# Optimization experiments

Measured on AMD Instinct MI355X. Metric: run time of the kernel, lower is better.

## Reference

```python
import jax, jax.numpy as jnp
import numpy as np

N = 1048576      # batch of 3D points
NT = 8           # n_transforms
HID = 64         # hidden_dim
NB = 12          # num_bins
TB = 5.0         # tail_bound
MINW = 1e-3
MINH = 1e-3
MIND = 1e-3
OUT_DIM = 2 * NB * 3 + 2   # 74, per repo's out_features formula (37 per transformed feature)
DCONST = float(np.log(np.exp(1.0 - MIND) - 1.0))  # softplus^-1(1 - min_derivative)
LOGZ = -0.5 * 3.0 * float(np.log(2.0 * np.pi))


def setup_inputs() -> dict:
    key = jax.random.key(0)
    k = jax.random.split(key, 7)
    x = jax.random.normal(k[0], (N, 3), jnp.float32)
    # ResidualNet params per coupling layer (stacked over NT layers):
    W_in = jax.random.normal(k[1], (NT, HID, 1)) * 0.5
    b_in = jax.random.normal(k[2], (NT, HID)) * 0.1
    W_blk = jax.random.normal(k[3], (NT, 4, HID, HID)) * (1.0 / np.sqrt(HID))
    b_blk = jax.random.normal(k[4], (NT, 4, HID)) * 0.1
    W_out = jax.random.normal(k[5], (NT, OUT_DIM, HID)) * 0.1
    b_out = jax.random.normal(k[6], (NT, OUT_DIM)) * 0.1
    return dict(x=x, W_in=W_in, b_in=b_in, W_blk=W_blk, b_blk=b_blk,
                W_out=W_out, b_out=b_out)


def _knots(unnorm, min_size):
    # softmax -> min-width floor -> cumulative knot positions on [-TB, TB]
    sizes = jax.nn.softmax(unnorm, axis=-1)
    sizes = min_size + (1.0 - min_size * NB) * sizes
    cum = jnp.cumsum(sizes, axis=-1)
    cum = jnp.pad(cum, ((0, 0), (0, 0), (1, 0)))
    cum = 2.0 * TB * cum - TB
    cum = cum.at[..., 0].set(-TB).at[..., -1].set(TB)
    return cum, cum[..., 1:] - cum[..., :-1]


def _rq_spline(x, uw, uh, ud):
    # x: [N,2]; uw,uh: [N,2,NB]; ud: [N,2,NB+1]  (extra derivative param, as in repo)
    inside = (x >= -TB) & (x <= TB)
    xc = jnp.clip(x, -TB, TB)
    cw, widths = _knots(uw, MINW)
    ch, heights = _knots(uh, MINH)
    ud_p = jnp.pad(ud, ((0, 0), (0, 0), (1, 1)), constant_values=DCONST)
    d = MIND + jax.nn.softplus(ud_p)   # [N,2,NB+3]; knots 0..NB used
    # searchsorted: sum(x >= edges) - 1, with eps on last edge (nflows convention)
    cw_s = cw.at[..., -1].add(1e-6)
    bin_idx = jnp.sum((xc[..., None] >= cw_s).astype(jnp.int32), axis=-1) - 1
    bin_idx = jnp.clip(bin_idx, 0, NB - 1)
    idx = bin_idx[..., None]

    def g(a, i):
        return jnp.take_along_axis(a, i, axis=-1)[..., 0]

    in_cw = g(cw, idx)
    in_w = g(widths, idx)
    in_ch = g(ch, idx)
    in_h = g(heights, idx)
    delta = in_h / in_w
    d_k = g(d, idx)
    d_k1 = g(d, idx + 1)

    theta = (xc - in_cw) / in_w
    t1m = theta * (1.0 - theta)
    numerator = in_h * (delta * theta * theta + d_k * t1m)
    denominator = delta + (d_k + d_k1 - 2.0 * delta) * t1m
    y = in_ch + numerator / denominator
    dnum = (delta * delta) * (d_k1 * theta * theta + 2.0 * delta * t1m
                              + d_k * (1.0 - theta) ** 2)
    lad = jnp.log(dnum) - 2.0 * jnp.log(denominator)
    return jnp.where(inside, y, x), jnp.where(inside, lad, 0.0)


def reference(x, W_in, b_in, W_blk, b_blk, W_out, b_out):
    z = x
    lad_total = jnp.zeros(x.shape[0], x.dtype)
    for i in range(NT):
        z = z[:, ::-1]                       # ReversePermutation(features=3)
        ident, tr = z[:, :1], z[:, 1:]       # mask [0,1,1]: feat 0 identity, 1&2 transformed
        # ResidualNet: initial linear, 2 pre-activation residual blocks, final linear
        h = ident @ W_in[i].T + b_in[i]
        for j in range(2):
            t = jax.nn.relu(h) @ W_blk[i, 2 * j].T + b_blk[i, 2 * j]
            t = jax.nn.relu(t) @ W_blk[i, 2 * j + 1].T + b_blk[i, 2 * j + 1]
            h = h + t
        params = (h @ W_out[i].T + b_out[i]).reshape(-1, 2, 3 * NB + 1)
        uw = params[..., :NB]
        uh = params[..., NB:2 * NB]
        ud = params[..., 2 * NB:]
        tr_new, lad = _rq_spline(tr, uw, uh, ud)
        lad_total = lad_total + lad.sum(axis=-1)
        z = jnp.concatenate([ident, tr_new], axis=1)
    return -0.5 * jnp.sum(z * z, axis=-1) + LOGZ + lad_total
```

## Files before the change

kernel.cpp:

```cpp
#include <hip/hip_runtime.h>
#include <math.h>

namespace {

constexpr int   NT_   = 8;
constexpr int   NB_   = 12;
constexpr float TB_   = 5.0f;
constexpr float MINW_ = 0.001f;
constexpr float MINH_ = 0.001f;
constexpr float MIND_ = 0.001f;
constexpr float LOGZ_ = -2.7568155996140185f;

constexpr int PPP_   = 41;
constexpr int WAVES_ = 4;

constexpr int WT_DENSE_F = 32 * 4096;
constexpr int HEAD_FB    = WT_DENSE_F;
constexpr int WT_HEAD_F  = 8 * 5120;
constexpr int PREP_TOT_F = WT_DENSE_F + WT_HEAD_F;

constexpr int P2B_       = 131072;
constexpr int WT_P2      = 32 * 2048;
constexpr int HEAD_PB    = P2B_ + WT_P2;
constexpr int HP2B_      = HEAD_PB + WT_HEAD_F;
constexpr int WT_HP2     = 8 * 2560;
constexpr int PREP_TOT_P = HP2B_ + WT_HP2;
constexpr size_t WS_P_BYTES = (size_t)PREP_TOT_P * 4;

typedef __attribute__((ext_vector_type(8))) short        bf16x8;
typedef __attribute__((ext_vector_type(4))) float        f32x4;
typedef __attribute__((ext_vector_type(4))) unsigned int u32x4;

__device__ __forceinline__ float softplus_(float v) {
    return fmaxf(v, 0.0f) + log1pf(__expf(-fabsf(v)));
}

__device__ __forceinline__ void rq_spline_reg(const float (&p)[37], float xr,
                                              float& y_out, float& lad_out) {
    float mw = -1e30f, mh = -1e30f;
#pragma unroll
    for (int q = 0; q < NB_; ++q) { mw = fmaxf(mw, p[q]); mh = fmaxf(mh, p[NB_ + q]); }

    float ew[NB_], eh[NB_];
    float sw = 0.0f, sh = 0.0f;
#pragma unroll
    for (int q = 0; q < NB_; ++q) { ew[q] = __expf(p[q] - mw);        sw += ew[q]; }
#pragma unroll
    for (int q = 0; q < NB_; ++q) { eh[q] = __expf(p[NB_ + q] - mh);  sh += eh[q]; }

    const float iw = (1.0f - MINW_ * (float)NB_) / sw;
    const float ih = (1.0f - MINH_ * (float)NB_) / sh;

    float cw[NB_ + 1], ch[NB_ + 1];
    cw[0] = -TB_; ch[0] = -TB_;
    float rw = 0.0f, rh = 0.0f;
#pragma unroll
    for (int q = 0; q < NB_; ++q) {
        rw += MINW_ + ew[q] * iw;
        rh += MINH_ + eh[q] * ih;
        cw[q + 1] = fmaf(2.0f * TB_, rw, -TB_);
        ch[q + 1] = fmaf(2.0f * TB_, rh, -TB_);
    }
    cw[NB_] = TB_;
    ch[NB_] = TB_;

    const float xc = fminf(fmaxf(xr, -TB_), TB_);

    int bi = 0;
#pragma unroll
    for (int q = 1; q <= NB_ - 1; ++q) bi += (xc >= cw[q]) ? 1 : 0;

    float in_cw = cw[0], cwn = cw[1], in_ch = ch[0], chn = ch[1];
    float udm1 = 0.0f, ud0 = p[24];
#pragma unroll
    for (int q = 1; q < NB_; ++q) {
        const bool s = (bi == q);
        in_cw = s ? cw[q]         : in_cw;
        cwn   = s ? cw[q + 1]     : cwn;
        in_ch = s ? ch[q]         : in_ch;
        chn   = s ? ch[q + 1]     : chn;
        udm1  = s ? p[24 + q - 1] : udm1;
        ud0   = s ? p[24 + q]     : ud0;
    }
    const float in_w = cwn - in_cw;
    const float in_h = chn - in_ch;
    const float d_k  = (bi == 0) ? 1.0f : (MIND_ + softplus_(udm1));
    const float d_k1 = MIND_ + softplus_(ud0);

    const float delta = in_h / in_w;
    const float theta = (xc - in_cw) / in_w;
    const float omt   = 1.0f - theta;
    const float t1m   = theta * omt;
    const float num   = in_h * (delta * theta * theta + d_k * t1m);
    const float den   = delta + (d_k + d_k1 - 2.0f * delta) * t1m;
    const float y     = in_ch + num / den;
    const float dnum  = delta * delta * (d_k1 * theta * theta + 2.0f * delta * t1m + d_k * omt * omt);
    const float lad   = __logf(dnum) - 2.0f * __logf(den);

    const bool inside = (xr >= -TB_) && (xr <= TB_);
    y_out   = inside ? y   : xr;
    lad_out = inside ? lad : 0.0f;
}

__device__ __forceinline__ float trunc16_(float x) {
    return __uint_as_float(__float_as_uint(x) & 0xFFFF0000u);
}
__device__ __forceinline__ unsigned hi16_(float x) { return __float_as_uint(x) >> 16; }

__device__ __forceinline__ int head_param_(int ctg, int c) {
    if (ctg < 2)  return ctg * 16 + c;
    if (ctg >= 3) return 37 + (ctg - 3) * 16 + c;
    if (c < 5)                 return 32 + c;
    if (c >= 8 && c < 13)      return 69 + (c - 8);
    return -1;
}

__global__ __launch_bounds__(256) void prep_F(const float* __restrict__ Wb,
                                              const float* __restrict__ Wo,
                                              float* __restrict__ wt) {
    const int t = blockIdx.x * 256 + threadIdx.x;
    if (t >= PREP_TOT_F) return;
    if (t < WT_DENSE_F) {
        const int L   = t >> 12;
        const int rem = t & 4095;
        const int o   = rem >> 6;
        const int q   = (rem >> 2) & 15;
        const int k   = ((q ^ (o & 15)) << 2) | (rem & 3);
        wt[t] = Wb[((size_t)L * 64 + o) * 64 + k];
    } else {
        const int t2  = t - WT_DENSE_F;
        const int i   = t2 / 5120;
        const int r1  = t2 - i * 5120;
        const int ctg = r1 >> 10;
        const int rem = r1 & 1023;
        const int c   = rem >> 6;
        const int q   = (rem >> 2) & 15;
        const int k   = ((q ^ c) << 2) | (rem & 3);
        const int param = head_param_(ctg, c);
        wt[t] = (param >= 0) ? Wo[((size_t)i * 74 + param) * 64 + k] : 0.0f;
    }
}

__global__ __launch_bounds__(256) void prep_P(const float* __restrict__ Wb,
                                              const float* __restrict__ Wo,
                                              float* __restrict__ wt) {
    const int t = blockIdx.x * 256 + threadIdx.x;
    if (t >= PREP_TOT_P) return;
    unsigned* wtu = (unsigned*)wt;
    if (t < WT_DENSE_F) {
        const int L   = t >> 12;
        const int rem = t & 4095;
        const int o   = rem >> 6;
        const int q   = (rem >> 2) & 15;
        const int k   = ((q ^ (o & 15)) << 2) | (rem & 3);
        const float x  = Wb[((size_t)L * 64 + o) * 64 + k];
        wtu[t] = (hi16_(x) << 16) | hi16_(x - trunc16_(x));
    } else if (t < HEAD_PB) {
        const int t2   = t - P2B_;
        const int L    = t2 >> 11;
        const int rem  = t2 & 2047;
        const int g    = rem >> 8;
        const int ct   = g >> 1, ks = g & 1;
        const int r    = rem & 255;
        const int lane = r >> 2, j = r & 3;
        const int o    = ct * 16 + (lane & 15);
        const int kb   = 32 * ks + 8 * (lane >> 4) + 2 * j;
        const float x0 = Wb[((size_t)L * 64 + o) * 64 + kb];
        const float x1 = Wb[((size_t)L * 64 + o) * 64 + kb + 1];
        const float a0 = x0 - trunc16_(x0), b0 = a0 - trunc16_(a0);
        const float a1 = x1 - trunc16_(x1), b1 = a1 - trunc16_(a1);
        wtu[t] = (hi16_(b1) << 16) | hi16_(b0);
    } else if (t < HP2B_) {
        const int t2  = t - HEAD_PB;
        const int i   = t2 / 5120;
        const int r1  = t2 - i * 5120;
        const int ctg = r1 >> 10;
        const int rem = r1 & 1023;
        const int c   = rem >> 6;
        const int q   = (rem >> 2) & 15;
        const int k   = ((q ^ c) << 2) | (rem & 3);
        const int param = head_param_(ctg, c);
        const float x = (param >= 0) ? Wo[((size_t)i * 74 + param) * 64 + k] : 0.0f;
        wtu[t] = (hi16_(x) << 16) | hi16_(x - trunc16_(x));
    } else {
        const int t2   = t - HP2B_;
        const int i    = t2 / 2560;
        const int r1   = t2 - i * 2560;
        const int ctg  = r1 >> 9;
        const int r2   = r1 & 511;
        const int ks   = r2 >> 8;
        const int r    = r2 & 255;
        const int lane = r >> 2, j = r & 3;
        const int c    = lane & 15;
        const int kb   = 32 * ks + 8 * (lane >> 4) + 2 * j;
        const int param = head_param_(ctg, c);
        float x0 = 0.0f, x1 = 0.0f;
        if (param >= 0) {
            x0 = Wo[((size_t)i * 74 + param) * 64 + kb];
            x1 = Wo[((size_t)i * 74 + param) * 64 + kb + 1];
        }
        const float a0 = x0 - trunc16_(x0), b0 = a0 - trunc16_(a0);
        const float a1 = x1 - trunc16_(x1), b1 = a1 - trunc16_(a1);
        wtu[t] = (hi16_(b1) << 16) | hi16_(b0);
    }
}

template <int NC>
__device__ __forceinline__ void stage_(const float* __restrict__ g, float* lds,
                                       int wave, int wl) {
#pragma unroll
    for (int c = 0; c < (NC + WAVES_ - 1) / WAVES_; ++c) {
        const int cc = wave + WAVES_ * c;
        if (cc < NC) {
            __builtin_amdgcn_global_load_lds(
                (const __attribute__((address_space(1))) void*)(g + cc * 256 + wl * 4),
                (__attribute__((address_space(3))) void*)(lds + cc * 256), 16, 0, 0);
        }
    }
}

__device__ __forceinline__ f32x4 mfma16(u32x4 a, u32x4 b, f32x4 c) {
    return __builtin_amdgcn_mfma_f32_16x16x32_bf16(
        __builtin_bit_cast(bf16x8, a), __builtin_bit_cast(bf16x8, b), c, 0, 0, 0);
}

__device__ __forceinline__ u32x4 packhi8(const float (&v)[8]) {
    u32x4 r;
    r.x = __builtin_amdgcn_perm(__float_as_uint(v[1]), __float_as_uint(v[0]), 0x07060302u);
    r.y = __builtin_amdgcn_perm(__float_as_uint(v[3]), __float_as_uint(v[2]), 0x07060302u);
    r.z = __builtin_amdgcn_perm(__float_as_uint(v[5]), __float_as_uint(v[4]), 0x07060302u);
    r.w = __builtin_amdgcn_perm(__float_as_uint(v[7]), __float_as_uint(v[6]), 0x07060302u);
    return r;
}

__device__ __forceinline__ void split3_8(const float (&xv)[8],
                                         u32x4& f0, u32x4& f1, u32x4& f2) {
    float r1[8], r2[8];
#pragma unroll
    for (int j = 0; j < 8; ++j) r1[j] = xv[j] - trunc16_(xv[j]);
#pragma unroll
    for (int j = 0; j < 8; ++j) r2[j] = r1[j] - trunc16_(r1[j]);
    f0 = packhi8(xv);
    f1 = packhi8(r1);
    f2 = packhi8(r2);
}

__device__ __forceinline__ void load3(const float* __restrict__ base, int tbase,
                                      int r1, int r2, u32x4& f0, u32x4& f1, u32x4& f2) {
    const f32x4 q0 = *(const f32x4*)&base[tbase + r1];
    const f32x4 q1 = *(const f32x4*)&base[tbase + r2];
    const float xv[8] = {q0.x, q0.y, q0.z, q0.w, q1.x, q1.y, q1.z, q1.w};
    split3_8(xv, f0, f1, f2);
}

__device__ __forceinline__ void unpack01(const unsigned* __restrict__ WsU, int tbase,
                                         int r1, int r2, u32x4& b0, u32x4& b1) {
    const u32x4 d0 = *(const u32x4*)&WsU[tbase + r1];
    const u32x4 d1 = *(const u32x4*)&WsU[tbase + r2];
    b0.x = __builtin_amdgcn_perm(d0.y, d0.x, 0x07060302u);
    b0.y = __builtin_amdgcn_perm(d0.w, d0.z, 0x07060302u);
    b0.z = __builtin_amdgcn_perm(d1.y, d1.x, 0x07060302u);
    b0.w = __builtin_amdgcn_perm(d1.w, d1.z, 0x07060302u);
    b1.x = __builtin_amdgcn_perm(d0.y, d0.x, 0x05040100u);
    b1.y = __builtin_amdgcn_perm(d0.w, d0.z, 0x05040100u);
    b1.z = __builtin_amdgcn_perm(d1.y, d1.x, 0x05040100u);
    b1.w = __builtin_amdgcn_perm(d1.w, d1.z, 0x05040100u);
}

__device__ __forceinline__ void loadA_all(const float* __restrict__ slab,
                                          const int (&R1v)[2], const int (&R2v)[2],
                                          u32x4 (&a0)[4][2], u32x4 (&a1)[4][2],
                                          u32x4 (&a2)[4][2]) {
#pragma unroll
    for (int ks = 0; ks < 2; ++ks)
#pragma unroll
        for (int rt = 0; rt < 4; ++rt)
            load3(slab, rt * 1024, R1v[ks], R2v[ks],
                  a0[rt][ks], a1[rt][ks], a2[rt][ks]);
}

__device__ __forceinline__ void chain6(const u32x4& A0, const u32x4& A1, const u32x4& A2,
                                       const u32x4& b0, const u32x4& b1, const u32x4& b2,
                                       f32x4& a) {
    a = mfma16(A0, b2, a);
    a = mfma16(A2, b0, a);
    a = mfma16(A1, b1, a);
    a = mfma16(A1, b0, a);
    a = mfma16(A0, b1, a);
    a = mfma16(A0, b0, a);
}

__device__ __forceinline__ void gemm_ct_F(const float* __restrict__ Ws, int ct,
                                          const u32x4 (&a0)[4][2], const u32x4 (&a1)[4][2],
                                          const u32x4 (&a2)[4][2],
                                          const int (&R1v)[2], const int (&R2v)[2],
                                          f32x4 (&acc)[4]) {
#pragma unroll
    for (int ks = 0; ks < 2; ++ks) {
        u32x4 b0, b1, b2;
        load3(Ws, ct * 1024, R1v[ks], R2v[ks], b0, b1, b2);
#pragma unroll
        for (int rt = 0; rt < 4; ++rt)
            chain6(a0[rt][ks], a1[rt][ks], a2[rt][ks], b0, b1, b2, acc[rt]);
    }
}

__device__ __forceinline__ void gemm_ct_P(const unsigned* __restrict__ WsU, int ct,
                                          const u32x4 (&a0)[4][2], const u32x4 (&a1)[4][2],
                                          const u32x4 (&a2)[4][2],
                                          const int (&R1v)[2], const int (&R2v)[2],
                                          const unsigned* __restrict__ p2t,
                                          f32x4 (&acc)[4]) {
    u32x4 b2[2];
#pragma unroll
    for (int ks = 0; ks < 2; ++ks)
        b2[ks] = *(const u32x4*)(p2t + ks * 256);
#pragma unroll
    for (int ks = 0; ks < 2; ++ks) {
        u32x4 b0, b1;
        unpack01(WsU, ct * 1024, R1v[ks], R2v[ks], b0, b1);
#pragma unroll
        for (int rt = 0; rt < 4; ++rt)
            chain6(a0[rt][ks], a1[rt][ks], a2[rt][ks], b0, b1, b2[ks], acc[rt]);
    }
}

template <bool P, bool RESID, bool RELU_OUT>
__device__ __forceinline__ void dense_layer(
    float* __restrict__ slab, const float* __restrict__ Ws,
    const u32x4 (&a0)[4][2], const u32x4 (&a1)[4][2], const u32x4 (&a2)[4][2],
    const int (&R1v)[2], const int (&R2v)[2],
    const unsigned* __restrict__ p2,
    const float* __restrict__ bias_g, float (&hreg)[4][4][4],
    const int (&K1)[4], const int (&K2)[4], int l15)
{
    const unsigned* WsU = (const unsigned*)Ws;
    float bly[4];
#pragma unroll
    for (int ct = 0; ct < 4; ++ct) bly[ct] = bias_g[ct * 16 + l15];
#pragma unroll
    for (int ct = 0; ct < 4; ++ct) {
        f32x4 acc[4];
#pragma unroll
        for (int rt = 0; rt < 4; ++rt) {
            if (RESID)
                acc[rt] = f32x4{hreg[rt][ct][0] + bly[ct], hreg[rt][ct][1] + bly[ct],
                                hreg[rt][ct][2] + bly[ct], hreg[rt][ct][3] + bly[ct]};
            else
                acc[rt] = f32x4{bly[ct], bly[ct], bly[ct], bly[ct]};
        }
        if constexpr (P)
            gemm_ct_P(WsU, ct, a0, a1, a2, R1v, R2v, p2 + ct * 512, acc);
        else
            gemm_ct_F(Ws, ct, a0, a1, a2, R1v, R2v, acc);
#pragma unroll
        for (int rt = 0; rt < 4; ++rt) {
            if (RESID) {
#pragma unroll
                for (int r = 0; r < 4; ++r) hreg[rt][ct][r] = acc[rt][r];
            }
            const int base = rt * 1024 + K2[ct];
#pragma unroll
            for (int r = 0; r < 4; ++r) {
                const float v = RELU_OUT ? fmaxf(acc[rt][r], 0.0f) : acc[rt][r];
                slab[base + K1[r]] = v;
            }
        }
    }
}

template <bool P>
__device__ __forceinline__ void head_ct(const float* __restrict__ Ws, int ct,
                                        const u32x4 (&a0)[4][2], const u32x4 (&a1)[4][2],
                                        const u32x4 (&a2)[4][2],
                                        const int (&R1v)[2], const int (&R2v)[2],
                                        const unsigned* __restrict__ hp2, int ctg,
                                        f32x4 (&acc)[4]) {
    if constexpr (P)
        gemm_ct_P((const unsigned*)Ws, ct, a0, a1, a2, R1v, R2v, hp2 + ctg * 512, acc);
    else
        gemm_ct_F(Ws, ct, a0, a1, a2, R1v, R2v, acc);
}

template <bool P>
__global__ __launch_bounds__(256, 2) void nsf_kernel(
    const float* __restrict__ x,
    const float* __restrict__ W_in,  const float* __restrict__ b_in,
    const float* __restrict__ b_blk, const float* __restrict__ b_out,
    const float* __restrict__ wt,
    float* __restrict__ out, int n)
{
    __shared__ __align__(16) float As2[WAVES_ * 4096];
    __shared__ __align__(16) float Ws[4096];

    constexpr int HB = P ? HEAD_PB : HEAD_FB;

    const int l    = threadIdx.x;
    const int wave = l >> 6;
    const int wl   = l & 63;
    const int l15  = wl & 15;
    const int lhi  = wl >> 4;
    float* slab = As2 + wave * 4096;

    const int gidx = blockIdx.x * 256 + l;
    const int idx  = gidx < n ? gidx : (n - 1);

    float z0 = x[3 * idx + 0];
    float z1 = x[3 * idx + 1];
    float z2 = x[3 * idx + 2];
    float lad_total = 0.0f;

    int K1[4], K2[4], R1v[2], R2v[2], P1[4];
#pragma unroll
    for (int r = 0; r < 4; ++r)
        K1[r] = (4 * lhi + r) * 64 + ((((l15 >> 2) ^ r)) << 2) + (l15 & 3);
#pragma unroll
    for (int c = 0; c < 4; ++c) K2[c] = (c ^ lhi) << 4;
#pragma unroll
    for (int s = 0; s < 2; ++s) {
        const int c0 = 8 * s + 2 * lhi;
        R1v[s] = l15 * 64 + ((c0 ^ l15) << 2);
        R2v[s] = l15 * 64 + (((c0 + 1) ^ l15) << 2);
    }
#pragma unroll
    for (int r = 0; r < 4; ++r) P1[r] = (4 * lhi + r) * PPP_ + l15;

    const unsigned* p2w  = (const unsigned*)wt + P2B_  + wl * 4;
    const unsigned* hp2w = (const unsigned*)wt + HP2B_ + wl * 4;

    stage_<16>(wt, Ws, wave, wl);
    __syncthreads();

#pragma unroll 1
    for (int i = 0; i < NT_; ++i) {
        const float ident = z2, tr0 = z1, tr1 = z0;
        const unsigned* hp2 = hp2w + (size_t)i * 2560;

        u32x4 a0[4][2], a1[4][2], a2[4][2];
        float hreg[4][4][4];
        {
            float idA[4], idD[4][4];
#pragma unroll
            for (int rt = 0; rt < 4; ++rt) idA[rt] = __shfl(ident, 16 * rt + l15, 64);
#pragma unroll
            for (int rt = 0; rt < 4; ++rt)
#pragma unroll
                for (int r = 0; r < 4; ++r)
                    idD[rt][r] = __shfl(ident, 16 * rt + 4 * lhi + r, 64);
#pragma unroll
            for (int ks = 0; ks < 2; ++ks) {
                const int kb = i * 64 + 32 * ks + 8 * lhi;
                const f32x4 w0 = *(const f32x4*)&W_in[kb];
                const f32x4 w1 = *(const f32x4*)&W_in[kb + 4];
                const f32x4 c0 = *(const f32x4*)&b_in[kb];
                const f32x4 c1 = *(const f32x4*)&b_in[kb + 4];
                const float wv[8] = {w0.x, w0.y, w0.z, w0.w, w1.x, w1.y, w1.z, w1.w};
                const float bv[8] = {c0.x, c0.y, c0.z, c0.w, c1.x, c1.y, c1.z, c1.w};
#pragma unroll
                for (int rt = 0; rt < 4; ++rt) {
                    float hx[8];
#pragma unroll
                    for (int j = 0; j < 8; ++j)
                        hx[j] = fmaxf(fmaf(idA[rt], wv[j], bv[j]), 0.0f);
                    split3_8(hx, a0[rt][ks], a1[rt][ks], a2[rt][ks]);
                }
            }
#pragma unroll
            for (int ct = 0; ct < 4; ++ct) {
                const float wD = W_in[i * 64 + ct * 16 + l15];
                const float bD = b_in[i * 64 + ct * 16 + l15];
#pragma unroll
                for (int rt = 0; rt < 4; ++rt)
#pragma unroll
                    for (int r = 0; r < 4; ++r)
                        hreg[rt][ct][r] = fmaf(idD[rt][r], wD, bD);
            }
        }

        dense_layer<P, false, true>(slab, Ws, a0, a1, a2, R1v, R2v,
                                    p2w + (size_t)(i * 4 + 0) * 2048,
                                    b_blk + (size_t)(i * 4 + 0) * 64, hreg, K1, K2, l15);
        __syncthreads();
        stage_<16>(wt + (size_t)(i * 4 + 1) * 4096, Ws, wave, wl);
        loadA_all(slab, R1v, R2v, a0, a1, a2);
        __syncthreads();

        dense_layer<P, true, true>(slab, Ws, a0, a1, a2, R1v, R2v,
                                   p2w + (size_t)(i * 4 + 1) * 2048,
                                   b_blk + (size_t)(i * 4 + 1) * 64, hreg, K1, K2, l15);
        __syncthreads();
        stage_<16>(wt + (size_t)(i * 4 + 2) * 4096, Ws, wave, wl);
        loadA_all(slab, R1v, R2v, a0, a1, a2);
        __syncthreads();

        dense_layer<P, false, true>(slab, Ws, a0, a1, a2, R1v, R2v,
                                    p2w + (size_t)(i * 4 + 2) * 2048,
                                    b_blk + (size_t)(i * 4 + 2) * 64, hreg, K1, K2, l15);
        __syncthreads();
        stage_<16>(wt + (size_t)(i * 4 + 3) * 4096, Ws, wave, wl);
        loadA_all(slab, R1v, R2v, a0, a1, a2);
        __syncthreads();

        dense_layer<P, true, false>(slab, Ws, a0, a1, a2, R1v, R2v,
                                    p2w + (size_t)(i * 4 + 3) * 2048,
                                    b_blk + (size_t)(i * 4 + 3) * 64, hreg, K1, K2, l15);
        __syncthreads();
        stage_<12>(wt + HB + (size_t)i * 5120, Ws, wave, wl);
        loadA_all(slab, R1v, R2v, a0, a1, a2);
        __syncthreads();

        f32x4 combD[4];
#pragma unroll
        for (int ct = 0; ct < 3; ++ct) {
            f32x4 acc[4];
#pragma unroll
            for (int rt = 0; rt < 4; ++rt) acc[rt] = f32x4{0.f, 0.f, 0.f, 0.f};
            head_ct<P>(Ws, ct, a0, a1, a2, R1v, R2v, hp2, ct, acc);
            if (ct < 2) {
#pragma unroll
                for (int rt = 0; rt < 4; ++rt)
#pragma unroll
                    for (int r = 0; r < 4; ++r)
                        slab[rt * 656 + P1[r] + 16 * ct] = acc[rt][r];
            } else {
#pragma unroll
                for (int rt = 0; rt < 4; ++rt) combD[rt] = acc[rt];
                if (l15 < 5) {
#pragma unroll
                    for (int rt = 0; rt < 4; ++rt)
#pragma unroll
                        for (int r = 0; r < 4; ++r)
                            slab[rt * 656 + P1[r] + 32] = acc[rt][r];
                }
            }
        }
        __syncthreads();
        stage_<8>(wt + HB + (size_t)i * 5120 + 3072, Ws, wave, wl);

        const float* bo = b_out + i * 74;
        float y0, l0v, y1, l1v;
        {
            float p0[37];
#pragma unroll
            for (int q = 0; q < 37; ++q) p0[q] = slab[wl * PPP_ + q] + bo[q];
            rq_spline_reg(p0, tr0, y0, l0v);
        }
        __syncthreads();

#pragma unroll
        for (int ct = 0; ct < 2; ++ct) {
            f32x4 acc[4];
#pragma unroll
            for (int rt = 0; rt < 4; ++rt) acc[rt] = f32x4{0.f, 0.f, 0.f, 0.f};
            head_ct<P>(Ws, ct, a0, a1, a2, R1v, R2v, hp2, 3 + ct, acc);
#pragma unroll
            for (int rt = 0; rt < 4; ++rt)
#pragma unroll
                for (int r = 0; r < 4; ++r)
                    slab[rt * 656 + P1[r] + 16 * ct] = acc[rt][r];
        }
        if (l15 >= 8 && l15 < 13) {
#pragma unroll
            for (int rt = 0; rt < 4; ++rt)
#pragma unroll
                for (int r = 0; r < 4; ++r)
                    slab[rt * 656 + P1[r] + 24] = combD[rt][r];
        }
        __syncthreads();
        if (i < NT_ - 1) stage_<16>(wt + (size_t)((i + 1) * 4) * 4096, Ws, wave, wl);
        {
            float p1[37];
#pragma unroll
            for (int q = 0; q < 37; ++q) p1[q] = slab[wl * PPP_ + q] + bo[37 + q];
            rq_spline_reg(p1, tr1, y1, l1v);
        }
        __syncthreads();

        lad_total += l0v + l1v;
        z0 = ident;
        z1 = y0;
        z2 = y1;
    }

    if (gidx < n)
        out[gidx] = -0.5f * (z0 * z0 + z1 * z1 + z2 * z2) + LOGZ_ + lad_total;
}

}

extern "C" void kernel_launch(void* const* d_in, const int* in_sizes, int n_in,
                              void* d_out, int out_size, void* d_ws, size_t ws_size,
                              hipStream_t stream) {
    const float* x     = (const float*)d_in[0];
    const float* W_in  = (const float*)d_in[1];
    const float* b_in  = (const float*)d_in[2];
    const float* W_blk = (const float*)d_in[3];
    const float* b_blk = (const float*)d_in[4];
    const float* W_out = (const float*)d_in[5];
    const float* b_out = (const float*)d_in[6];
    float* out = (float*)d_out;

    const int n = in_sizes[0] / 3;
    const int grid = (n + 255) / 256;

    if (ws_size >= WS_P_BYTES) {
        prep_P<<<(PREP_TOT_P + 255) / 256, 256, 0, stream>>>(
            W_blk, W_out, (float*)d_ws);
        nsf_kernel<true><<<grid, 256, 0, stream>>>(x, W_in, b_in, b_blk, b_out,
                                                   (const float*)d_ws, out, n);
    } else {
        prep_F<<<(PREP_TOT_F + 255) / 256, 256, 0, stream>>>(
            W_blk, W_out, (float*)d_ws);
        nsf_kernel<false><<<grid, 256, 0, stream>>>(x, W_in, b_in, b_blk, b_out,
                                                    (const float*)d_ws, out, n);
    }
}
```

Measured before the change: 1.880 ms.

## Read MFMA B-fragments directly from global in per-lane layout, drop LDS weight staging

The packed weight path is reorganised so the dense and head weights are pre-permuted into per-lane fragment order. Each wave then loads its B operands straight from global memory (L2-cached), so the LDS weight staging and block-wide barriers go away. The kernel becomes single-wave blocks (64 threads, launch_bounds 64,3) with a per-wave LDS slab, which can raise occupancy and remove synchronisation. The trade-off is more global/L2 traffic for weights, since each wave re-reads them instead of sharing them through LDS.

```diff
diff --git a/kernel.cpp b/kernel.cpp
--- a/kernel.cpp
+++ b/kernel.cpp
@@ -141,18 +141,24 @@
     }
 }
 
-__global__ __launch_bounds__(256) void prep_P(const float* __restrict__ Wb,
+__global__ __launch_bounds__(256) void prep_G(const float* __restrict__ Wb,
                                               const float* __restrict__ Wo,
                                               float* __restrict__ wt) {
     const int t = blockIdx.x * 256 + threadIdx.x;
     if (t >= PREP_TOT_P) return;
     unsigned* wtu = (unsigned*)wt;
     if (t < WT_DENSE_F) {
-        const int L   = t >> 12;
-        const int rem = t & 4095;
-        const int o   = rem >> 6;
-        const int q   = (rem >> 2) & 15;
-        const int k   = ((q ^ (o & 15)) << 2) | (rem & 3);
+        const int L    = t >> 12;
+        const int rem  = t & 4095;
+        const int ct   = rem >> 10;
+        const int r2   = rem & 1023;
+        const int ks   = r2 >> 9;
+        const int r3   = r2 & 511;
+        const int half = r3 >> 8;
+        const int r4   = r3 & 255;
+        const int lane = r4 >> 2, m = r4 & 3;
+        const int o    = ct * 16 + (lane & 15);
+        const int k    = ks * 32 + (lane >> 4) * 8 + half * 4 + m;
         const float x  = Wb[((size_t)L * 64 + o) * 64 + k];
         wtu[t] = (hi16_(x) << 16) | hi16_(x - trunc16_(x));
     } else if (t < HEAD_PB) {
@@ -171,14 +177,18 @@
         const float a1 = x1 - trunc16_(x1), b1 = a1 - trunc16_(a1);
         wtu[t] = (hi16_(b1) << 16) | hi16_(b0);
     } else if (t < HP2B_) {
-        const int t2  = t - HEAD_PB;
-        const int i   = t2 / 5120;
-        const int r1  = t2 - i * 5120;
-        const int ctg = r1 >> 10;
-        const int rem = r1 & 1023;
-        const int c   = rem >> 6;
-        const int q   = (rem >> 2) & 15;
-        const int k   = ((q ^ c) << 2) | (rem & 3);
+        const int t2   = t - HEAD_PB;
+        const int i    = t2 / 5120;
+        const int r1   = t2 - i * 5120;
+        const int ctg  = r1 >> 10;
+        const int r2   = r1 & 1023;
+        const int ks   = r2 >> 9;
+        const int r3   = r2 & 511;
+        const int half = r3 >> 8;
+        const int r4   = r3 & 255;
+        const int lane = r4 >> 2, m = r4 & 3;
+        const int c    = lane & 15;
+        const int k    = ks * 32 + (lane >> 4) * 8 + half * 4 + m;
         const int param = head_param_(ctg, c);
         const float x = (param >= 0) ? Wo[((size_t)i * 74 + param) * 64 + k] : 0.0f;
         wtu[t] = (hi16_(x) << 16) | hi16_(x - trunc16_(x));
@@ -253,10 +263,8 @@
     split3_8(xv, f0, f1, f2);
 }
 
-__device__ __forceinline__ void unpack01(const unsigned* __restrict__ WsU, int tbase,
-                                         int r1, int r2, u32x4& b0, u32x4& b1) {
-    const u32x4 d0 = *(const u32x4*)&WsU[tbase + r1];
-    const u32x4 d1 = *(const u32x4*)&WsU[tbase + r2];
+__device__ __forceinline__ void unpack01r(const u32x4& d0, const u32x4& d1,
+                                          u32x4& b0, u32x4& b1) {
     b0.x = __builtin_amdgcn_perm(d0.y, d0.x, 0x07060302u);
     b0.y = __builtin_amdgcn_perm(d0.w, d0.z, 0x07060302u);
     b0.z = __builtin_amdgcn_perm(d1.y, d1.x, 0x07060302u);
@@ -305,36 +313,37 @@
     }
 }
 
-__device__ __forceinline__ void gemm_ct_P(const unsigned* __restrict__ WsU, int ct,
+__device__ __forceinline__ void gemm_ct_G(const unsigned* __restrict__ p01t,
+                                          const unsigned* __restrict__ p2t,
                                           const u32x4 (&a0)[4][2], const u32x4 (&a1)[4][2],
                                           const u32x4 (&a2)[4][2],
-                                          const int (&R1v)[2], const int (&R2v)[2],
-                                          const unsigned* __restrict__ p2t,
                                           f32x4 (&acc)[4]) {
-    u32x4 b2[2];
-#pragma unroll
-    for (int ks = 0; ks < 2; ++ks)
-        b2[ks] = *(const u32x4*)(p2t + ks * 256);
+    u32x4 d0[2], d1[2], c2[2];
+#pragma unroll
+    for (int ks = 0; ks < 2; ++ks) {
+        d0[ks] = *(const u32x4*)(p01t + ks * 512);
+        d1[ks] = *(const u32x4*)(p01t + ks * 512 + 256);
+        c2[ks] = *(const u32x4*)(p2t + ks * 256);
+    }
 #pragma unroll
     for (int ks = 0; ks < 2; ++ks) {
         u32x4 b0, b1;
-        unpack01(WsU, ct * 1024, R1v[ks], R2v[ks], b0, b1);
+        unpack01r(d0[ks], d1[ks], b0, b1);
 #pragma unroll
         for (int rt = 0; rt < 4; ++rt)
-            chain6(a0[rt][ks], a1[rt][ks], a2[rt][ks], b0, b1, b2[ks], acc[rt]);
-    }
-}
-
-template <bool P, bool RESID, bool RELU_OUT>
-__device__ __forceinline__ void dense_layer(
-    float* __restrict__ slab, const float* __restrict__ Ws,
+            chain6(a0[rt][ks], a1[rt][ks], a2[rt][ks], b0, b1, c2[ks], acc[rt]);
+    }
+}
+
+template <bool RESID, bool RELU_OUT>
+__device__ __forceinline__ void dense_layer_G(
+    float* __restrict__ slab,
     const u32x4 (&a0)[4][2], const u32x4 (&a1)[4][2], const u32x4 (&a2)[4][2],
-    const int (&R1v)[2], const int (&R2v)[2],
+    const unsigned* __restrict__ p01,
     const unsigned* __restrict__ p2,
     const float* __restrict__ bias_g, float (&hreg)[4][4][4],
     const int (&K1)[4], const int (&K2)[4], int l15)
 {
-    const unsigned* WsU = (const unsigned*)Ws;
     float bly[4];
 #pragma unroll
     for (int ct = 0; ct < 4; ++ct) bly[ct] = bias_g[ct * 16 + l15];
@@ -349,10 +358,7 @@
             else
                 acc[rt] = f32x4{bly[ct], bly[ct], bly[ct], bly[ct]};
         }
-        if constexpr (P)
-            gemm_ct_P(WsU, ct, a0, a1, a2, R1v, R2v, p2 + ct * 512, acc);
-        else
-            gemm_ct_F(Ws, ct, a0, a1, a2, R1v, R2v, acc);
+        gemm_ct_G(p01 + ct * 1024, p2 + ct * 512, a0, a1, a2, acc);
 #pragma unroll
         for (int rt = 0; rt < 4; ++rt) {
             if (RESID) {
@@ -369,21 +375,233 @@
     }
 }
 
-template <bool P>
-__device__ __forceinline__ void head_ct(const float* __restrict__ Ws, int ct,
-                                        const u32x4 (&a0)[4][2], const u32x4 (&a1)[4][2],
-                                        const u32x4 (&a2)[4][2],
-                                        const int (&R1v)[2], const int (&R2v)[2],
-                                        const unsigned* __restrict__ hp2, int ctg,
-                                        f32x4 (&acc)[4]) {
-    if constexpr (P)
-        gemm_ct_P((const unsigned*)Ws, ct, a0, a1, a2, R1v, R2v, hp2 + ctg * 512, acc);
-    else
+__device__ __forceinline__ void h_init_(int i, float ident, int l15, int lhi,
+                                        const float* __restrict__ W_in,
+                                        const float* __restrict__ b_in,
+                                        u32x4 (&a0)[4][2], u32x4 (&a1)[4][2],
+                                        u32x4 (&a2)[4][2], float (&hreg)[4][4][4]) {
+    float idA[4], idD[4][4];
+#pragma unroll
+    for (int rt = 0; rt < 4; ++rt) idA[rt] = __shfl(ident, 16 * rt + l15, 64);
+#pragma unroll
+    for (int rt = 0; rt < 4; ++rt)
+#pragma unroll
+        for (int r = 0; r < 4; ++r)
+            idD[rt][r] = __shfl(ident, 16 * rt + 4 * lhi + r, 64);
+#pragma unroll
+    for (int ks = 0; ks < 2; ++ks) {
+        const int kb = i * 64 + 32 * ks + 8 * lhi;
+        const f32x4 w0 = *(const f32x4*)&W_in[kb];
+        const f32x4 w1 = *(const f32x4*)&W_in[kb + 4];
+        const f32x4 c0 = *(const f32x4*)&b_in[kb];
+        const f32x4 c1 = *(const f32x4*)&b_in[kb + 4];
+        const float wv[8] = {w0.x, w0.y, w0.z, w0.w, w1.x, w1.y, w1.z, w1.w};
+        const float bv[8] = {c0.x, c0.y, c0.z, c0.w, c1.x, c1.y, c1.z, c1.w};
+#pragma unroll
+        for (int rt = 0; rt < 4; ++rt) {
+            float hx[8];
+#pragma unroll
+            for (int j = 0; j < 8; ++j)
+                hx[j] = fmaxf(fmaf(idA[rt], wv[j], bv[j]), 0.0f);
+            split3_8(hx, a0[rt][ks], a1[rt][ks], a2[rt][ks]);
+        }
+    }
+#pragma unroll
+    for (int ct = 0; ct < 4; ++ct) {
+        const float wD = W_in[i * 64 + ct * 16 + l15];
+        const float bD = b_in[i * 64 + ct * 16 + l15];
+#pragma unroll
+        for (int rt = 0; rt < 4; ++rt)
+#pragma unroll
+            for (int r = 0; r < 4; ++r)
+                hreg[rt][ct][r] = fmaf(idD[rt][r], wD, bD);
+    }
+}
+
+__global__ __launch_bounds__(64, 3) void nsf_g(
+    const float* __restrict__ x,
+    const float* __restrict__ W_in,  const float* __restrict__ b_in,
+    const float* __restrict__ b_blk, const float* __restrict__ b_out,
+    const float* __restrict__ wt,
+    float* __restrict__ out, int n)
+{
+    __shared__ __align__(16) float slab[4096];
+
+    const int wl  = threadIdx.x;
+    const int l15 = wl & 15;
+    const int lhi = wl >> 4;
+
+    const int gidx = blockIdx.x * 64 + wl;
+    const int idx  = gidx < n ? gidx : (n - 1);
+
+    float z0 = x[3 * idx + 0];
+    float z1 = x[3 * idx + 1];
+    float z2 = x[3 * idx + 2];
+    float lad_total = 0.0f;
+
+    int K1[4], K2[4], R1v[2], R2v[2], P1[4];
+#pragma unroll
+    for (int r = 0; r < 4; ++r)
+        K1[r] = (4 * lhi + r) * 64 + ((((l15 >> 2) ^ r)) << 2) + (l15 & 3);
+#pragma unroll
+    for (int c = 0; c < 4; ++c) K2[c] = (c ^ lhi) << 4;
+#pragma unroll
+    for (int s = 0; s < 2; ++s) {
+        const int c0 = 8 * s + 2 * lhi;
+        R1v[s] = l15 * 64 + ((c0 ^ l15) << 2);
+        R2v[s] = l15 * 64 + (((c0 + 1) ^ l15) << 2);
+    }
+#pragma unroll
+    for (int r = 0; r < 4; ++r) P1[r] = (4 * lhi + r) * PPP_ + l15;
+
+    const unsigned* b01w  = (const unsigned*)wt +           wl * 4;
+    const unsigned* p2w   = (const unsigned*)wt + P2B_    + wl * 4;
+    const unsigned* hb01w = (const unsigned*)wt + HEAD_PB + wl * 4;
+    const unsigned* hp2w  = (const unsigned*)wt + HP2B_   + wl * 4;
+
+#pragma unroll 1
+    for (int i = 0; i < NT_; ++i) {
+        const float ident = z2, tr0 = z1, tr1 = z0;
+
+        u32x4 a0[4][2], a1[4][2], a2[4][2];
+        float hreg[4][4][4];
+        h_init_(i, ident, l15, lhi, W_in, b_in, a0, a1, a2, hreg);
+
+        dense_layer_G<false, true>(slab, a0, a1, a2,
+                                   b01w + (size_t)(i * 4 + 0) * 4096,
+                                   p2w  + (size_t)(i * 4 + 0) * 2048,
+                                   b_blk + (size_t)(i * 4 + 0) * 64, hreg, K1, K2, l15);
+        loadA_all(slab, R1v, R2v, a0, a1, a2);
+        dense_layer_G<true, true>(slab, a0, a1, a2,
+                                  b01w + (size_t)(i * 4 + 1) * 4096,
+                                  p2w  + (size_t)(i * 4 + 1) * 2048,
+                                  b_blk + (size_t)(i * 4 + 1) * 64, hreg, K1, K2, l15);
+        loadA_all(slab, R1v, R2v, a0, a1, a2);
+        dense_layer_G<false, true>(slab, a0, a1, a2,
+                                   b01w + (size_t)(i * 4 + 2) * 4096,
+                                   p2w  + (size_t)(i * 4 + 2) * 2048,
+                                   b_blk + (size_t)(i * 4 + 2) * 64, hreg, K1, K2, l15);
+        loadA_all(slab, R1v, R2v, a0, a1, a2);
+        dense_layer_G<true, false>(slab, a0, a1, a2,
+                                   b01w + (size_t)(i * 4 + 3) * 4096,
+                                   p2w  + (size_t)(i * 4 + 3) * 2048,
+                                   b_blk + (size_t)(i * 4 + 3) * 64, hreg, K1, K2, l15);
+        loadA_all(slab, R1v, R2v, a0, a1, a2);
+
+        const unsigned* hb01 = hb01w + (size_t)i * 5120;
+        const unsigned* hp2  = hp2w  + (size_t)i * 2560;
+
+        f32x4 combD[4];
+#pragma unroll
+        for (int ct = 0; ct < 3; ++ct) {
+            f32x4 acc[4];
+#pragma unroll
+            for (int rt = 0; rt < 4; ++rt) acc[rt] = f32x4{0.f, 0.f, 0.f, 0.f};
+            gemm_ct_G(hb01 + ct * 1024, hp2 + ct * 512, a0, a1, a2, acc);
+            if (ct < 2) {
+#pragma unroll
+                for (int rt = 0; rt < 4; ++rt)
+#pragma unroll
+                    for (int r = 0; r < 4; ++r)
+                        slab[rt * 656 + P1[r] + 16 * ct] = acc[rt][r];
+            } else {
+#pragma unroll
+                for (int rt = 0; rt < 4; ++rt) combD[rt] = acc[rt];
+                if (l15 < 5) {
+#pragma unroll
+                    for (int rt = 0; rt < 4; ++rt)
+#pragma unroll
+                        for (int r = 0; r < 4; ++r)
+                            slab[rt * 656 + P1[r] + 32] = acc[rt][r];
+                }
+            }
+        }
+
+        const float* bo = b_out + i * 74;
+        float y0, l0v, y1, l1v;
+        {
+            float p0[37];
+#pragma unroll
+            for (int q = 0; q < 37; ++q) p0[q] = slab[wl * PPP_ + q] + bo[q];
+            rq_spline_reg(p0, tr0, y0, l0v);
+        }
+
+#pragma unroll
+        for (int ct = 0; ct < 2; ++ct) {
+            f32x4 acc[4];
+#pragma unroll
+            for (int rt = 0; rt < 4; ++rt) acc[rt] = f32x4{0.f, 0.f, 0.f, 0.f};
+            gemm_ct_G(hb01 + (3 + ct) * 1024, hp2 + (3 + ct) * 512, a0, a1, a2, acc);
+#pragma unroll
+            for (int rt = 0; rt < 4; ++rt)
+#pragma unroll
+                for (int r = 0; r < 4; ++r)
+                    slab[rt * 656 + P1[r] + 16 * ct] = acc[rt][r];
+        }
+        if (l15 >= 8 && l15 < 13) {
+#pragma unroll
+            for (int rt = 0; rt < 4; ++rt)
+#pragma unroll
+                for (int r = 0; r < 4; ++r)
+                    slab[rt * 656 + P1[r] + 24] = combD[rt][r];
+        }
+        {
+            float p1[37];
+#pragma unroll
+            for (int q = 0; q < 37; ++q) p1[q] = slab[wl * PPP_ + q] + bo[37 + q];
+            rq_spline_reg(p1, tr1, y1, l1v);
+        }
+
+        lad_total += l0v + l1v;
+        z0 = ident;
+        z1 = y0;
+        z2 = y1;
+    }
+
+    if (gidx < n)
+        out[gidx] = -0.5f * (z0 * z0 + z1 * z1 + z2 * z2) + LOGZ_ + lad_total;
+}
+
+template <bool RESID, bool RELU_OUT>
+__device__ __forceinline__ void dense_layer_F(
+    float* __restrict__ slab, const float* __restrict__ Ws,
+    const u32x4 (&a0)[4][2], const u32x4 (&a1)[4][2], const u32x4 (&a2)[4][2],
+    const int (&R1v)[2], const int (&R2v)[2],
+    const float* __restrict__ bias_g, float (&hreg)[4][4][4],
+    const int (&K1)[4], const int (&K2)[4], int l15)
+{
+    float bly[4];
+#pragma unroll
+    for (int ct = 0; ct < 4; ++ct) bly[ct] = bias_g[ct * 16 + l15];
+#pragma unroll
+    for (int ct = 0; ct < 4; ++ct) {
+        f32x4 acc[4];
+#pragma unroll
+        for (int rt = 0; rt < 4; ++rt) {
+            if (RESID)
+                acc[rt] = f32x4{hreg[rt][ct][0] + bly[ct], hreg[rt][ct][1] + bly[ct],
+                                hreg[rt][ct][2] + bly[ct], hreg[rt][ct][3] + bly[ct]};
+            else
+                acc[rt] = f32x4{bly[ct], bly[ct], bly[ct], bly[ct]};
+        }
         gemm_ct_F(Ws, ct, a0, a1, a2, R1v, R2v, acc);
-}
-
-template <bool P>
-__global__ __launch_bounds__(256, 2) void nsf_kernel(
+#pragma unroll
+        for (int rt = 0; rt < 4; ++rt) {
+            if (RESID) {
+#pragma unroll
+                for (int r = 0; r < 4; ++r) hreg[rt][ct][r] = acc[rt][r];
+            }
+            const int base = rt * 1024 + K2[ct];
+#pragma unroll
+            for (int r = 0; r < 4; ++r) {
+                const float v = RELU_OUT ? fmaxf(acc[rt][r], 0.0f) : acc[rt][r];
+                slab[base + K1[r]] = v;
+            }
+        }
+    }
+}
+
+__global__ __launch_bounds__(256, 2) void nsf_f(
     const float* __restrict__ x,
     const float* __restrict__ W_in,  const float* __restrict__ b_in,
     const float* __restrict__ b_blk, const float* __restrict__ b_out,
@@ -393,8 +611,6 @@
     __shared__ __align__(16) float As2[WAVES_ * 4096];
     __shared__ __align__(16) float Ws[4096];
 
-    constexpr int HB = P ? HEAD_PB : HEAD_FB;
-
     const int l    = threadIdx.x;
     const int wave = l >> 6;
     const int wl   = l & 63;
@@ -425,87 +641,42 @@
 #pragma unroll
     for (int r = 0; r < 4; ++r) P1[r] = (4 * lhi + r) * PPP_ + l15;
 
-    const unsigned* p2w  = (const unsigned*)wt + P2B_  + wl * 4;
-    const unsigned* hp2w = (const unsigned*)wt + HP2B_ + wl * 4;
-
     stage_<16>(wt, Ws, wave, wl);
     __syncthreads();
 
 #pragma unroll 1
     for (int i = 0; i < NT_; ++i) {
         const float ident = z2, tr0 = z1, tr1 = z0;
-        const unsigned* hp2 = hp2w + (size_t)i * 2560;
 
         u32x4 a0[4][2], a1[4][2], a2[4][2];
         float hreg[4][4][4];
-        {
-            float idA[4], idD[4][4];
-#pragma unroll
-            for (int rt = 0; rt < 4; ++rt) idA[rt] = __shfl(ident, 16 * rt + l15, 64);
-#pragma unroll
-            for (int rt = 0; rt < 4; ++rt)
-#pragma unroll
-                for (int r = 0; r < 4; ++r)
-                    idD[rt][r] = __shfl(ident, 16 * rt + 4 * lhi + r, 64);
-#pragma unroll
-            for (int ks = 0; ks < 2; ++ks) {
-                const int kb = i * 64 + 32 * ks + 8 * lhi;
-                const f32x4 w0 = *(const f32x4*)&W_in[kb];
-                const f32x4 w1 = *(const f32x4*)&W_in[kb + 4];
-                const f32x4 c0 = *(const f32x4*)&b_in[kb];
-                const f32x4 c1 = *(const f32x4*)&b_in[kb + 4];
-                const float wv[8] = {w0.x, w0.y, w0.z, w0.w, w1.x, w1.y, w1.z, w1.w};
-                const float bv[8] = {c0.x, c0.y, c0.z, c0.w, c1.x, c1.y, c1.z, c1.w};
-#pragma unroll
-                for (int rt = 0; rt < 4; ++rt) {
-                    float hx[8];
-#pragma unroll
-                    for (int j = 0; j < 8; ++j)
-                        hx[j] = fmaxf(fmaf(idA[rt], wv[j], bv[j]), 0.0f);
-                    split3_8(hx, a0[rt][ks], a1[rt][ks], a2[rt][ks]);
-                }
-            }
-#pragma unroll
-            for (int ct = 0; ct < 4; ++ct) {
-                const float wD = W_in[i * 64 + ct * 16 + l15];
-                const float bD = b_in[i * 64 + ct * 16 + l15];
-#pragma unroll
-                for (int rt = 0; rt < 4; ++rt)
-#pragma unroll
-                    for (int r = 0; r < 4; ++r)
-                        hreg[rt][ct][r] = fmaf(idD[rt][r], wD, bD);
-            }
-        }
-
-        dense_layer<P, false, true>(slab, Ws, a0, a1, a2, R1v, R2v,
-                                    p2w + (size_t)(i * 4 + 0) * 2048,
-                                    b_blk + (size_t)(i * 4 + 0) * 64, hreg, K1, K2, l15);
+        h_init_(i, ident, l15, lhi, W_in, b_in, a0, a1, a2, hreg);
+
+        dense_layer_F<false, true>(slab, Ws, a0, a1, a2, R1v, R2v,
+                                   b_blk + (size_t)(i * 4 + 0) * 64, hreg, K1, K2, l15);
         __syncthreads();
         stage_<16>(wt + (size_t)(i * 4 + 1) * 4096, Ws, wave, wl);
         loadA_all(slab, R1v, R2v, a0, a1, a2);
         __syncthreads();
 
-        dense_layer<P, true, true>(slab, Ws, a0, a1, a2, R1v, R2v,
-                                   p2w + (size_t)(i * 4 + 1) * 2048,
-                                   b_blk + (size_t)(i * 4 + 1) * 64, hreg, K1, K2, l15);
+        dense_layer_F<true, true>(slab, Ws, a0, a1, a2, R1v, R2v,
+                                  b_blk + (size_t)(i * 4 + 1) * 64, hreg, K1, K2, l15);
         __syncthreads();
         stage_<16>(wt + (size_t)(i * 4 + 2) * 4096, Ws, wave, wl);
         loadA_all(slab, R1v, R2v, a0, a1, a2);
         __syncthreads();
 
-        dense_layer<P, false, true>(slab, Ws, a0, a1, a2, R1v, R2v,
-                                    p2w + (size_t)(i * 4 + 2) * 2048,
-                                    b_blk + (size_t)(i * 4 + 2) * 64, hreg, K1, K2, l15);
+        dense_layer_F<false, true>(slab, Ws, a0, a1, a2, R1v, R2v,
+                                   b_blk + (size_t)(i * 4 + 2) * 64, hreg, K1, K2, l15);
         __syncthreads();
         stage_<16>(wt + (size_t)(i * 4 + 3) * 4096, Ws, wave, wl);
         loadA_all(slab, R1v, R2v, a0, a1, a2);
         __syncthreads();
 
-        dense_layer<P, true, false>(slab, Ws, a0, a1, a2, R1v, R2v,
-                                    p2w + (size_t)(i * 4 + 3) * 2048,
-                                    b_blk + (size_t)(i * 4 + 3) * 64, hreg, K1, K2, l15);
-        __syncthreads();
-        stage_<12>(wt + HB + (size_t)i * 5120, Ws, wave, wl);
+        dense_layer_F<true, false>(slab, Ws, a0, a1, a2, R1v, R2v,
+                                   b_blk + (size_t)(i * 4 + 3) * 64, hreg, K1, K2, l15);
+        __syncthreads();
+        stage_<12>(wt + HEAD_FB + (size_t)i * 5120, Ws, wave, wl);
         loadA_all(slab, R1v, R2v, a0, a1, a2);
         __syncthreads();
 
@@ -515,7 +686,7 @@
             f32x4 acc[4];
 #pragma unroll
             for (int rt = 0; rt < 4; ++rt) acc[rt] = f32x4{0.f, 0.f, 0.f, 0.f};
-            head_ct<P>(Ws, ct, a0, a1, a2, R1v, R2v, hp2, ct, acc);
+            gemm_ct_F(Ws, ct, a0, a1, a2, R1v, R2v, acc);
             if (ct < 2) {
 #pragma unroll
                 for (int rt = 0; rt < 4; ++rt)
@@ -535,7 +706,7 @@
             }
         }
         __syncthreads();
-        stage_<8>(wt + HB + (size_t)i * 5120 + 3072, Ws, wave, wl);
+        stage_<8>(wt + HEAD_FB + (size_t)i * 5120 + 3072, Ws, wave, wl);
 
         const float* bo = b_out + i * 74;
         float y0, l0v, y1, l1v;
@@ -552,7 +723,7 @@
             f32x4 acc[4];
 #pragma unroll
             for (int rt = 0; rt < 4; ++rt) acc[rt] = f32x4{0.f, 0.f, 0.f, 0.f};
-            head_ct<P>(Ws, ct, a0, a1, a2, R1v, R2v, hp2, 3 + ct, acc);
+            gemm_ct_F(Ws, ct, a0, a1, a2, R1v, R2v, acc);
 #pragma unroll
             for (int rt = 0; rt < 4; ++rt)
 #pragma unroll
@@ -601,17 +772,18 @@
     float* out = (float*)d_out;
 
     const int n = in_sizes[0] / 3;
-    const int grid = (n + 255) / 256;
 
     if (ws_size >= WS_P_BYTES) {
-        prep_P<<<(PREP_TOT_P + 255) / 256, 256, 0, stream>>>(
+        prep_G<<<(PREP_TOT_P + 255) / 256, 256, 0, stream>>>(
             W_blk, W_out, (float*)d_ws);
-        nsf_kernel<true><<<grid, 256, 0, stream>>>(x, W_in, b_in, b_blk, b_out,
-                                                   (const float*)d_ws, out, n);
+        const int grid = (n + 63) / 64;
+        nsf_g<<<grid, 64, 0, stream>>>(x, W_in, b_in, b_blk, b_out,
+                                       (const float*)d_ws, out, n);
     } else {
         prep_F<<<(PREP_TOT_F + 255) / 256, 256, 0, stream>>>(
             W_blk, W_out, (float*)d_ws);
-        nsf_kernel<false><<<grid, 256, 0, stream>>>(x, W_in, b_in, b_blk, b_out,
-                                                    (const float*)d_ws, out, n);
-    }
-}
+        const int grid = (n + 255) / 256;
+        nsf_f<<<grid, 256, 0, stream>>>(x, W_in, b_in, b_blk, b_out,
+                                        (const float*)d_ws, out, n);
+    }
+}
```

Result: slower. 3.624 ms (+92.8%).
